# Optimization experiments

Hardware: AMD Instinct MI355X
Metric: run time of the kernel (lower is better)

The kernel has to match this reference:

```python
import jax, jax.numpy as jnp
import numpy as np

B, N, H, W, C = 512, 16, 84, 84, 3
CNN_OUT, ATTN, GH, HEADS, POS, A_DIM = 256, 64, 128, 2, 3, 3
IN_GAT = CNN_OUT + POS  # 259
FLAT = 64 * 16 * 16     # conv output flat dim for 84x84 input


def setup_inputs() -> dict:
    key = jax.random.key(0)
    ks = jax.random.split(key, 16)
    s = 0.05
    return dict(
        cam=jax.random.uniform(ks[0], (B, H, W, C), jnp.float32),
        pos=jax.random.normal(ks[1], (B, POS), jnp.float32),
        team_pos=jax.random.normal(ks[2], (B, N, POS), jnp.float32) * 10.0,
        agent_idx=jax.random.randint(ks[3], (B,), 0, N),
        W1=jax.random.normal(ks[4], (32, C, 8, 8), jnp.float32) * s, b1=jnp.zeros((32,), jnp.float32),
        W2=jax.random.normal(ks[5], (64, 32, 4, 4), jnp.float32) * s, b2=jnp.zeros((64,), jnp.float32),
        W3=jax.random.normal(ks[6], (64, 64, 3, 3), jnp.float32) * s, b3=jnp.zeros((64,), jnp.float32),
        Wp=jax.random.normal(ks[7], (FLAT, CNN_OUT), jnp.float32) * 0.01, bp=jnp.zeros((CNN_OUT,), jnp.float32),
        Wid=jax.random.normal(ks[8], (1, ATTN), jnp.float32) * s, bid=jnp.zeros((ATTN,), jnp.float32),
        Wg=jax.random.normal(ks[9], (IN_GAT, HEADS * GH), jnp.float32) * s,
        a_src=jax.random.normal(ks[10], (HEADS, GH), jnp.float32) * s,
        a_dst=jax.random.normal(ks[11], (HEADS, GH), jnp.float32) * s,
        Wh1=jax.random.normal(ks[12], (HEADS * GH + ATTN, 256), jnp.float32) * s, bh1=jnp.zeros((256,), jnp.float32),
        Wh2=jax.random.normal(ks[13], (256, 2 * A_DIM), jnp.float32) * s, bh2=jnp.zeros((2 * A_DIM,), jnp.float32),
    )


def _conv(x, w, b, stride):
    y = jax.lax.conv_general_dilated(x, w, (stride, stride), 'VALID',
                                     dimension_numbers=('NCHW', 'OIHW', 'NCHW'))
    return jax.nn.relu(y + b[None, :, None, None])


def reference(cam, pos, team_pos, agent_idx, W1, b1, W2, b2, W3, b3, Wp, bp,
              Wid, bid, Wg, a_src, a_dst, Wh1, bh1, Wh2, bh2):
    # CNN encoder (NHWC -> NCHW)
    x = jnp.transpose(cam, (0, 3, 1, 2))
    x = _conv(x, W1, b1, 2)   # [B,32,39,39]
    x = _conv(x, W2, b2, 2)   # [B,64,18,18]
    x = _conv(x, W3, b3, 1)   # [B,64,16,16]
    cam_feat = jax.nn.relu(x.reshape(x.shape[0], -1) @ Wp + bp)  # [B,256]

    # per-node features: broadcast ego cam feat + relative team positions
    rel_pos = team_pos - pos[:, None, :]                                     # [B,N,3]
    node_feats = jnp.concatenate(
        [jnp.broadcast_to(cam_feat[:, None, :], (B, N, CNN_OUT)), rel_pos], axis=-1)  # [B,N,259]

    # adjacency: within 100m, no self-loops, self-loop added for isolated nodes
    dist = jnp.linalg.norm(team_pos[:, :, None, :] - team_pos[:, None, :, :], axis=-1)  # [B,N,N]
    eye = jnp.eye(N, dtype=node_feats.dtype)
    adj = (dist < 100.0).astype(node_feats.dtype) * (1.0 - eye)
    need_self = (adj.sum(axis=2) == 0).astype(adj.dtype)                     # [B,N]
    adj = adj + eye[None] * need_self[..., None]

    # dense multi-head GAT layer
    hN = (node_feats @ Wg).reshape(B, N, HEADS, GH)                          # [B,N,H,D]
    src = jnp.einsum('bnhd,hd->bnh', hN, a_src)
    dst = jnp.einsum('bnhd,hd->bnh', hN, a_dst)
    e = jax.nn.leaky_relu(src[:, :, None, :] + dst[:, None, :, :], 0.2)      # [B,i,j,H]
    e = jnp.where(adj[..., None] > 0, e, -1e9)
    alpha = jax.nn.softmax(e, axis=2)
    h = jnp.einsum('bijh,bjhd->bihd', alpha, hN).reshape(B, N, HEADS * GH)   # [B,N,256]
    h = jax.nn.elu(h)
    h = jnp.nan_to_num(h, nan=0.0, posinf=0.0, neginf=0.0)

    # agent-id embedding, fuse, gather own node, policy head
    id_emb = jax.nn.relu(agent_idx.astype(jnp.float32)[:, None] @ Wid + bid)  # [B,64]
    fused = jnp.concatenate([h, jnp.broadcast_to(id_emb[:, None, :], (B, N, ATTN))], axis=-1)  # [B,N,320]
    agent_feat = fused[jnp.arange(B), agent_idx]                             # [B,320]
    z = jax.nn.relu(agent_feat @ Wh1 + bh1)
    logits = z @ Wh2 + bh2                                                    # [B,6]
    return logits
```

## Files before the change

kernel.cpp:

```cpp
#include <hip/hip_runtime.h>


typedef __attribute__((ext_vector_type(8))) short bf16x8;
typedef __attribute__((ext_vector_type(4))) float f32x4;

union U4 { uint4 v; unsigned int u[4]; bf16x8 h; };

__device__ __forceinline__ unsigned short f2bf(float x) {
    unsigned int u = __float_as_uint(x);
    return (unsigned short)((u + 0x7FFFu + ((u >> 16) & 1u)) >> 16);
}
__device__ __forceinline__ unsigned int pack2(float lo, float hi) {
    return (unsigned int)f2bf(lo) | ((unsigned int)f2bf(hi) << 16);
}
__device__ __forceinline__ bf16x8 loadA(const unsigned int* __restrict__ W, int k8, int M, int oc) {
    U4 r; r.v = *(const uint4*)(W + (((size_t)k8 * M + oc) << 2));
    return r.h;
}
__device__ __forceinline__ bf16x8 loadB(const unsigned int* __restrict__ p, size_t BC) {
    U4 r; r.u[0] = p[0]; r.u[1] = p[BC]; r.u[2] = p[2 * BC]; r.u[3] = p[3 * BC];
    return r.h;
}
#define MFMA(a, b, c) __builtin_amdgcn_mfma_f32_16x16x32_bf16((a), (b), (c), 0, 0, 0)

__device__ __forceinline__ int xcd_swz(int L, int nwg) {
    int q = nwg >> 3, r = nwg & 7;
    int x = L & 7, i = L >> 3;
    return (x < r ? x * (q + 1) : r * (q + 1) + (x - r) * q) + i;
}

__global__ __launch_bounds__(256) void prepack(
    const float* __restrict__ W1, const float* __restrict__ W2,
    const float* __restrict__ W3, const float* __restrict__ Wp,
    const float* __restrict__ Wg, const float* __restrict__ Wh1,
    unsigned int* __restrict__ W1t, unsigned int* __restrict__ W2t,
    unsigned int* __restrict__ W3t, unsigned int* __restrict__ Wpt,
    unsigned int* __restrict__ Wgt, unsigned int* __restrict__ Wh1t)
{
    int i = blockIdx.x * 256 + threadIdx.x;
    if (i < 3072) {
        int j2 = i & 3, oc = (i >> 2) & 31, k8 = i >> 7;
        int c = k8 >> 3, kh = k8 & 7, kw = 2 * j2;
        const float* s = W1 + ((oc * 3 + c) * 8 + kh) * 8;
        W1t[i] = pack2(s[kw], s[kw + 1]);
    } else if (i < 19456) {
        int j = i - 3072;
        int j2 = j & 3, oc = (j >> 2) & 63, k8 = j >> 8;
        int tap = k8 >> 2, ic = (k8 & 3) * 8 + 2 * j2;
        int kh = tap >> 2, kw = tap & 3;
        float a = W2[((oc * 32 + ic) * 4 + kh) * 4 + kw];
        float b = W2[((oc * 32 + ic + 1) * 4 + kh) * 4 + kw];
        W2t[j] = pack2(a, b);
    } else if (i < 37888) {
        int j = i - 19456;
        int j2 = j & 3, oc = (j >> 2) & 63, k8 = j >> 8;
        int tap = k8 >> 3, ic = (k8 & 7) * 8 + 2 * j2;
        int kh = tap / 3, kw = tap % 3;
        float a = W3[((oc * 64 + ic) * 3 + kh) * 3 + kw];
        float b = W3[((oc * 64 + ic + 1) * 3 + kh) * 3 + kw];
        W3t[j] = pack2(a, b);
    } else if (i < 2135040) {
        int j = i - 37888;
        int j2 = j & 3, n = (j >> 2) & 255, k8 = j >> 10;
        int s3 = k8 >> 3, oc = (k8 & 7) * 8 + 2 * j2;
        float a = Wp[(size_t)(oc * 256 + s3) * 256 + n];
        float b = Wp[(size_t)((oc + 1) * 256 + s3) * 256 + n];
        Wpt[j] = pack2(a, b);
    } else if (i < 2167808) {
        int j = i - 2135040;
        int j2 = j & 3, m = (j >> 2) & 255, k8 = j >> 10;
        int k = k8 * 8 + 2 * j2;
        Wgt[j] = pack2(Wg[k * 256 + m], Wg[(k + 1) * 256 + m]);
    } else if (i < 2208768) {
        int j = i - 2167808;
        int j2 = j & 3, m = (j >> 2) & 255, k8 = j >> 10;
        int k = k8 * 8 + 2 * j2;
        Wh1t[j] = pack2(Wh1[k * 256 + m], Wh1[(k + 1) * 256 + m]);
    }
}

__global__ __launch_bounds__(256) void transpose_cam(
    const float* __restrict__ cam, unsigned int* __restrict__ camt, int b0, int BC)
{
    __shared__ float lds[32][253];
    int yy = blockIdx.x;
    int bb = blockIdx.y * 32;
    int t = threadIdx.x;
    for (int f = t; f < 8064; f += 256) {
        int b = f / 252, p = f - b * 252;
        lds[b][p] = cam[(size_t)(b0 + bb + b) * 21168 + yy * 252 + p];
    }
    __syncthreads();
    for (int g = t; g < 4032; g += 256) {
        int b = g & 31, q = g >> 5;
        int c = q / 42, x2 = q - c * 42;
        unsigned int v = pack2(lds[b][6 * x2 + c], lds[b][6 * x2 + 3 + c]);
        camt[(size_t)((c * 84 + yy) * 42 + x2) * BC + bb + b] = v;
    }
}

__global__ __launch_bounds__(256) void conv1_mfma(
    const unsigned int* __restrict__ in32, const unsigned int* __restrict__ Wt,
    const float* __restrict__ bias, unsigned int* __restrict__ out32, int BC, int bqShift)
{
    int wgid = xcd_swz(blockIdx.x, gridDim.x);
    int bq = wgid & ((1 << bqShift) - 1);
    int s = wgid >> bqShift;
    int oh = s / 39, ow = s - oh * 39;
    int wv = threadIdx.x >> 6, l = threadIdx.x & 63;
    int lg = l >> 4, lc = l & 15;
    const size_t sBC = (size_t)BC;
    size_t bcol = (size_t)bq * 128 + wv * 32 + lc;
    f32x4 acc[2][2] = {};
    int ybase = 2 * oh;
    #pragma unroll
    for (int sp = 0; sp < 3; sp++) {
        const int s0 = 2 * sp, s1 = s0 + 1;
        bf16x8 A0[2], A1[2], B0[2], B1[2];
        #pragma unroll
        for (int m = 0; m < 2; m++) {
            A0[m] = loadA(Wt, s0 * 4 + lg, 32, m * 16 + lc);
            A1[m] = loadA(Wt, s1 * 4 + lg, 32, m * 16 + lc);
        }
        const unsigned int* p0 = in32 + (size_t)((sp * 84 + ybase + lg) * 42 + ow) * sBC + bcol;
        const unsigned int* p1 = in32 + (size_t)((sp * 84 + ybase + 4 + lg) * 42 + ow) * sBC + bcol;
        B0[0] = loadB(p0, sBC); B0[1] = loadB(p0 + 16, sBC);
        B1[0] = loadB(p1, sBC); B1[1] = loadB(p1 + 16, sBC);
        #pragma unroll
        for (int m = 0; m < 2; m++) {
            acc[m][0] = MFMA(A0[m], B0[0], acc[m][0]);
            acc[m][1] = MFMA(A0[m], B0[1], acc[m][1]);
            acc[m][0] = MFMA(A1[m], B1[0], acc[m][0]);
            acc[m][1] = MFMA(A1[m], B1[1], acc[m][1]);
        }
    }
    #pragma unroll
    for (int m = 0; m < 2; m++) {
        float4 bv = *(const float4*)(bias + m * 16 + lg * 4);
        #pragma unroll
        for (int g = 0; g < 2; g++) {
            f32x4 a = acc[m][g];
            unsigned int u0 = pack2(fmaxf(a.x + bv.x, 0.f), fmaxf(a.y + bv.y, 0.f));
            unsigned int u1 = pack2(fmaxf(a.z + bv.z, 0.f), fmaxf(a.w + bv.w, 0.f));
            size_t o = (size_t)(s * 16 + m * 8 + lg * 2) * sBC
                     + (size_t)bq * 128 + wv * 32 + g * 16 + lc;
            out32[o] = u0; out32[o + sBC] = u1;
        }
    }
}

__global__ __launch_bounds__(256) void conv2_mfma(
    const unsigned int* __restrict__ in32, const unsigned int* __restrict__ Wt,
    const float* __restrict__ bias, unsigned int* __restrict__ out32, int BC, int bqShift)
{
    int wgid = xcd_swz(blockIdx.x, gridDim.x);
    int bq = wgid & ((1 << bqShift) - 1);
    int s = wgid >> bqShift;
    int oh = s / 18, ow = s - oh * 18;
    int wv = threadIdx.x >> 6, l = threadIdx.x & 63;
    int lg = l >> 4, lc = l & 15;
    const size_t sBC = (size_t)BC;
    size_t bcol = (size_t)bq * 128 + wv * 32 + lc;
    f32x4 acc[4][2] = {};
    int ybase = 2 * oh, xbase = 2 * ow;
    #pragma unroll
    for (int sp = 0; sp < 8; sp++) {
        const int s0 = 2 * sp, s1 = s0 + 1;
        bf16x8 A0[4], A1[4], B0[2], B1[2];
        #pragma unroll
        for (int m = 0; m < 4; m++) {
            A0[m] = loadA(Wt, s0 * 4 + lg, 64, m * 16 + lc);
            A1[m] = loadA(Wt, s1 * 4 + lg, 64, m * 16 + lc);
        }
        {
            const int kh = s0 >> 2, kw = s0 & 3;
            const unsigned int* p = in32
                + (size_t)((((ybase + kh) * 39 + xbase + kw) * 16) + lg * 4) * sBC + bcol;
            B0[0] = loadB(p, sBC); B0[1] = loadB(p + 16, sBC);
        }
        {
            const int kh = s1 >> 2, kw = s1 & 3;
            const unsigned int* p = in32
                + (size_t)((((ybase + kh) * 39 + xbase + kw) * 16) + lg * 4) * sBC + bcol;
            B1[0] = loadB(p, sBC); B1[1] = loadB(p + 16, sBC);
        }
        #pragma unroll
        for (int m = 0; m < 4; m++) {
            acc[m][0] = MFMA(A0[m], B0[0], acc[m][0]);
            acc[m][1] = MFMA(A0[m], B0[1], acc[m][1]);
        }
        #pragma unroll
        for (int m = 0; m < 4; m++) {
            acc[m][0] = MFMA(A1[m], B1[0], acc[m][0]);
            acc[m][1] = MFMA(A1[m], B1[1], acc[m][1]);
        }
    }
    #pragma unroll
    for (int m = 0; m < 4; m++) {
        float4 bv = *(const float4*)(bias + m * 16 + lg * 4);
        #pragma unroll
        for (int g = 0; g < 2; g++) {
            f32x4 a = acc[m][g];
            unsigned int u0 = pack2(fmaxf(a.x + bv.x, 0.f), fmaxf(a.y + bv.y, 0.f));
            unsigned int u1 = pack2(fmaxf(a.z + bv.z, 0.f), fmaxf(a.w + bv.w, 0.f));
            size_t o = (size_t)(s * 32 + m * 8 + lg * 2) * sBC
                     + (size_t)bq * 128 + wv * 32 + g * 16 + lc;
            out32[o] = u0; out32[o + sBC] = u1;
        }
    }
}

__global__ __launch_bounds__(256) void conv3_mfma(
    const unsigned int* __restrict__ in32, const unsigned int* __restrict__ Wt,
    const float* __restrict__ bias, unsigned int* __restrict__ out32, int BC, int bqShift)
{
    int wgid = xcd_swz(blockIdx.x, gridDim.x);
    int bq = wgid & ((1 << bqShift) - 1);
    int s = wgid >> bqShift;
    int oh = s >> 4, ow = s & 15;
    int wv = threadIdx.x >> 6, l = threadIdx.x & 63;
    int lg = l >> 4, lc = l & 15;
    const size_t sBC = (size_t)BC;
    size_t bcol = (size_t)bq * 128 + wv * 32 + lc;
    f32x4 acc[4][2] = {};
    #pragma unroll
    for (int sp = 0; sp < 9; sp++) {
        const int s0 = 2 * sp, s1 = s0 + 1;
        const int kh = sp / 3, kw = sp - kh * 3;
        bf16x8 A0[4], A1[4], B0[2], B1[2];
        #pragma unroll
        for (int m = 0; m < 4; m++) {
            A0[m] = loadA(Wt, s0 * 4 + lg, 64, m * 16 + lc);
            A1[m] = loadA(Wt, s1 * 4 + lg, 64, m * 16 + lc);
        }
        const unsigned int* pb = in32 + (size_t)((((oh + kh) * 18 + ow + kw) * 32)) * sBC;
        const unsigned int* p0 = pb + (size_t)(lg * 4) * sBC + bcol;
        const unsigned int* p1 = pb + (size_t)((4 + lg) * 4) * sBC + bcol;
        B0[0] = loadB(p0, sBC); B0[1] = loadB(p0 + 16, sBC);
        B1[0] = loadB(p1, sBC); B1[1] = loadB(p1 + 16, sBC);
        #pragma unroll
        for (int m = 0; m < 4; m++) {
            acc[m][0] = MFMA(A0[m], B0[0], acc[m][0]);
            acc[m][1] = MFMA(A0[m], B0[1], acc[m][1]);
        }
        #pragma unroll
        for (int m = 0; m < 4; m++) {
            acc[m][0] = MFMA(A1[m], B1[0], acc[m][0]);
            acc[m][1] = MFMA(A1[m], B1[1], acc[m][1]);
        }
    }
    #pragma unroll
    for (int m = 0; m < 4; m++) {
        float4 bv = *(const float4*)(bias + m * 16 + lg * 4);
        #pragma unroll
        for (int g = 0; g < 2; g++) {
            f32x4 a = acc[m][g];
            unsigned int u0 = pack2(fmaxf(a.x + bv.x, 0.f), fmaxf(a.y + bv.y, 0.f));
            unsigned int u1 = pack2(fmaxf(a.z + bv.z, 0.f), fmaxf(a.w + bv.w, 0.f));
            size_t o = (size_t)(s * 32 + m * 8 + lg * 2) * sBC
                     + (size_t)bq * 128 + wv * 32 + g * 16 + lc;
            out32[o] = u0; out32[o + sBC] = u1;
        }
    }
}

__global__ __launch_bounds__(256) void proj_mfma(
    const unsigned int* __restrict__ x3, const unsigned int* __restrict__ Wpt,
    float* __restrict__ partial, int BC, int bqShift)
{
    int wgid = xcd_swz(blockIdx.x, gridDim.x);
    int bq = wgid & ((1 << bqShift) - 1);
    int rem = wgid >> bqShift;
    int mq = rem & 3;
    int kseg = rem >> 2;
    int wv = threadIdx.x >> 6, l = threadIdx.x & 63;
    int lg = l >> 4, lc = l & 15;
    const size_t sBC = (size_t)BC;
    size_t bcol = (size_t)bq * 128 + wv * 32 + lc;
    f32x4 acc[4][2] = {};
    #pragma unroll
    for (int sp = 0; sp < 8; sp++) {
        const int s0 = 2 * sp, s1 = s0 + 1;
        const int s3 = kseg * 8 + sp;
        bf16x8 A0[4], A1[4], B0[2], B1[2];
        #pragma unroll
        for (int m = 0; m < 4; m++) {
            A0[m] = loadA(Wpt, kseg * 64 + s0 * 4 + lg, 256, mq * 64 + m * 16 + lc);
            A1[m] = loadA(Wpt, kseg * 64 + s1 * 4 + lg, 256, mq * 64 + m * 16 + lc);
        }
        const unsigned int* pb = x3 + (size_t)(s3 * 32) * sBC;
        const unsigned int* p0 = pb + (size_t)(lg * 4) * sBC + bcol;
        const unsigned int* p1 = pb + (size_t)((4 + lg) * 4) * sBC + bcol;
        B0[0] = loadB(p0, sBC); B0[1] = loadB(p0 + 16, sBC);
        B1[0] = loadB(p1, sBC); B1[1] = loadB(p1 + 16, sBC);
        #pragma unroll
        for (int m = 0; m < 4; m++) {
            acc[m][0] = MFMA(A0[m], B0[0], acc[m][0]);
            acc[m][1] = MFMA(A0[m], B0[1], acc[m][1]);
        }
        #pragma unroll
        for (int m = 0; m < 4; m++) {
            acc[m][0] = MFMA(A1[m], B1[0], acc[m][0]);
            acc[m][1] = MFMA(A1[m], B1[1], acc[m][1]);
        }
    }
    #pragma unroll
    for (int m = 0; m < 4; m++) {
        #pragma unroll
        for (int g = 0; g < 2; g++) {
            f32x4 a = acc[m][g];
            float* pp = partial
                + (size_t)(kseg * 256 + mq * 64 + m * 16 + lg * 4) * sBC
                + (size_t)bq * 128 + wv * 32 + g * 16 + lc;
            pp[0] = a.x; pp[sBC] = a.y; pp[2 * sBC] = a.z; pp[3 * sBC] = a.w;
        }
    }
}

__global__ __launch_bounds__(256) void reduce_k(
    const float* __restrict__ partial, const float* __restrict__ bp,
    unsigned int* __restrict__ cf16, int b0, int BC, int bcShift)
{
    int i = blockIdx.x * 256 + threadIdx.x;
    int bl = i & (BC - 1);
    int q = i >> bcShift;
    float s0 = 0.f, s1 = 0.f;
    int n0 = 2 * q;
    for (int seg = 0; seg < 32; seg++) {
        s0 += partial[((size_t)(seg * 256 + n0) << bcShift) + bl];
        s1 += partial[((size_t)(seg * 256 + n0 + 1) << bcShift) + bl];
    }
    float v0 = fmaxf(s0 + bp[n0], 0.f);
    float v1 = fmaxf(s1 + bp[n0 + 1], 0.f);
    cf16[(size_t)q * 512 + b0 + bl] = pack2(v0, v1);
}

__global__ __launch_bounds__(64) void gat_prep(
    const unsigned int* __restrict__ cf16, const unsigned int* __restrict__ Wgt,
    float* __restrict__ hNb)
{
    int mq = blockIdx.x, bq = blockIdx.y;
    int l = threadIdx.x, lg = l >> 4, lc = l & 15;
    size_t bcol = (size_t)bq * 32 + lc;
    f32x4 acc[4][2] = {};
    #pragma unroll
    for (int sp = 0; sp < 4; sp++) {
        const int s0 = 2 * sp, s1 = s0 + 1;
        bf16x8 A0[4], A1[4], B0[2], B1[2];
        #pragma unroll
        for (int m = 0; m < 4; m++) {
            A0[m] = loadA(Wgt, s0 * 4 + lg, 256, mq * 64 + m * 16 + lc);
            A1[m] = loadA(Wgt, s1 * 4 + lg, 256, mq * 64 + m * 16 + lc);
        }
        const unsigned int* p0 = cf16 + (size_t)(sp * 32 + lg * 4) * 512 + bcol;
        const unsigned int* p1 = p0 + (size_t)16 * 512;
        B0[0] = loadB(p0, 512); B0[1] = loadB(p0 + 16, 512);
        B1[0] = loadB(p1, 512); B1[1] = loadB(p1 + 16, 512);
        #pragma unroll
        for (int m = 0; m < 4; m++) {
            acc[m][0] = MFMA(A0[m], B0[0], acc[m][0]);
            acc[m][1] = MFMA(A0[m], B0[1], acc[m][1]);
        }
        #pragma unroll
        for (int m = 0; m < 4; m++) {
            acc[m][0] = MFMA(A1[m], B1[0], acc[m][0]);
            acc[m][1] = MFMA(A1[m], B1[1], acc[m][1]);
        }
    }
    #pragma unroll
    for (int m = 0; m < 4; m++) {
        #pragma unroll
        for (int g = 0; g < 2; g++) {
            size_t b = (size_t)bq * 32 + g * 16 + lc;
            int row0 = mq * 64 + m * 16 + lg * 4;
            *(f32x4*)(hNb + b * 256 + row0) = acc[m][g];
        }
    }
}

__global__ __launch_bounds__(256) void gat_mid(
    const float* __restrict__ hNb, const float* __restrict__ pos,
    const float* __restrict__ tpos, const int* __restrict__ aidx,
    const float* __restrict__ Wg, const float* __restrict__ asrc, const float* __restrict__ adst,
    const float* __restrict__ Wid, const float* __restrict__ bid,
    unsigned int* __restrict__ af16)
{
    int b = blockIdx.x, t = threadIdx.x;
    __shared__ float hN[16][256];
    __shared__ float srcv[16][2], dstv[16][2];
    __shared__ float alpha[16][2];
    __shared__ float af[320];
    __shared__ unsigned int adjm_s;

    int ai = aidx[b];
    float basev = hNb[(size_t)b * 256 + t];
    float rw0 = Wg[65536 + t], rw1 = Wg[65792 + t], rw2 = Wg[66048 + t];
    float px = pos[b * 3 + 0], py = pos[b * 3 + 1], pz = pos[b * 3 + 2];
    for (int n = 0; n < 16; n++) {
        float r0 = tpos[(b * 16 + n) * 3 + 0] - px;
        float r1 = tpos[(b * 16 + n) * 3 + 1] - py;
        float r2 = tpos[(b * 16 + n) * 3 + 2] - pz;
        hN[n][t] = basev + r0 * rw0 + r1 * rw1 + r2 * rw2;
    }

    if (t < 64) {
        bool on = false;
        if (t < 16 && t != ai) {
            float dx = tpos[(b * 16 + ai) * 3 + 0] - tpos[(b * 16 + t) * 3 + 0];
            float dy = tpos[(b * 16 + ai) * 3 + 1] - tpos[(b * 16 + t) * 3 + 1];
            float dz = tpos[(b * 16 + ai) * 3 + 2] - tpos[(b * 16 + t) * 3 + 2];
            on = (dx * dx + dy * dy + dz * dz) < 10000.0f;
        }
        unsigned long long m = __ballot(on);
        if (t == 0) adjm_s = (m == 0ull) ? (1u << ai) : (unsigned int)m;
    }
    __syncthreads();

    {
        int p = t >> 3, sub = t & 7;
        int j = p >> 1, h = p & 1;
        float s1 = 0.f, s2 = 0.f;
        #pragma unroll
        for (int dd = 0; dd < 16; dd++) {
            int d = h * 128 + sub * 16 + dd;
            float v = hN[j][d];
            s1 += v * asrc[d];
            s2 += v * adst[d];
        }
        s1 += __shfl_xor(s1, 1); s1 += __shfl_xor(s1, 2); s1 += __shfl_xor(s1, 4);
        s2 += __shfl_xor(s2, 1); s2 += __shfl_xor(s2, 2); s2 += __shfl_xor(s2, 4);
        if (sub == 0) { srcv[j][h] = s1; dstv[j][h] = s2; }
    }
    __syncthreads();

    if (t < 32) {
        int j = t & 15, h = t >> 4;
        unsigned int am = adjm_s;
        float e = srcv[ai][h] + dstv[j][h];
        e = (e > 0.f) ? e : 0.2f * e;
        e = ((am >> j) & 1u) ? e : -1e9f;
        float mx = e;
        mx = fmaxf(mx, __shfl_xor(mx, 1));
        mx = fmaxf(mx, __shfl_xor(mx, 2));
        mx = fmaxf(mx, __shfl_xor(mx, 4));
        mx = fmaxf(mx, __shfl_xor(mx, 8));
        float ex = __expf(e - mx);
        float sm = ex;
        sm += __shfl_xor(sm, 1); sm += __shfl_xor(sm, 2);
        sm += __shfl_xor(sm, 4); sm += __shfl_xor(sm, 8);
        alpha[j][h] = ex / sm;
    }
    __syncthreads();

    {
        int h = t >> 7;
        float o = 0.f;
        #pragma unroll
        for (int j = 0; j < 16; j++) o += alpha[j][h] * hN[j][t];
        o = (o > 0.f) ? o : (__expf(o) - 1.f);
        af[t] = o;
    }
    if (t < 64) {
        float v = (float)ai * Wid[t] + bid[t];
        af[256 + t] = fmaxf(v, 0.f);
    }
    __syncthreads();

    if (t < 160) af16[(size_t)t * 512 + b] = pack2(af[2 * t], af[2 * t + 1]);
}

__global__ __launch_bounds__(64) void head_mfma(
    const unsigned int* __restrict__ af16, const unsigned int* __restrict__ Wh1t,
    const float* __restrict__ bh1, float* __restrict__ zf)
{
    int mq = blockIdx.x, bq = blockIdx.y;
    int l = threadIdx.x, lg = l >> 4, lc = l & 15;
    size_t bcol = (size_t)bq * 32 + lc;
    f32x4 acc[4][2] = {};
    #pragma unroll
    for (int sp = 0; sp < 5; sp++) {
        const int s0 = 2 * sp, s1 = s0 + 1;
        bf16x8 A0[4], A1[4], B0[2], B1[2];
        #pragma unroll
        for (int m = 0; m < 4; m++) {
            A0[m] = loadA(Wh1t, s0 * 4 + lg, 256, mq * 64 + m * 16 + lc);
            A1[m] = loadA(Wh1t, s1 * 4 + lg, 256, mq * 64 + m * 16 + lc);
        }
        const unsigned int* p0 = af16 + (size_t)(sp * 32 + lg * 4) * 512 + bcol;
        const unsigned int* p1 = p0 + (size_t)16 * 512;
        B0[0] = loadB(p0, 512); B0[1] = loadB(p0 + 16, 512);
        B1[0] = loadB(p1, 512); B1[1] = loadB(p1 + 16, 512);
        #pragma unroll
        for (int m = 0; m < 4; m++) {
            acc[m][0] = MFMA(A0[m], B0[0], acc[m][0]);
            acc[m][1] = MFMA(A0[m], B0[1], acc[m][1]);
        }
        #pragma unroll
        for (int m = 0; m < 4; m++) {
            acc[m][0] = MFMA(A1[m], B1[0], acc[m][0]);
            acc[m][1] = MFMA(A1[m], B1[1], acc[m][1]);
        }
    }
    #pragma unroll
    for (int m = 0; m < 4; m++) {
        int row0 = mq * 64 + m * 16 + lg * 4;
        float4 bv = *(const float4*)(bh1 + row0);
        #pragma unroll
        for (int g = 0; g < 2; g++) {
            f32x4 a = acc[m][g];
            size_t b = (size_t)bq * 32 + g * 16 + lc;
            float* pp = zf + (size_t)row0 * 512 + b;
            pp[0]        = fmaxf(a.x + bv.x, 0.f);
            pp[512]      = fmaxf(a.y + bv.y, 0.f);
            pp[2 * 512]  = fmaxf(a.z + bv.z, 0.f);
            pp[3 * 512]  = fmaxf(a.w + bv.w, 0.f);
        }
    }
}

__global__ __launch_bounds__(256) void logits_k(
    const float* __restrict__ zf, const float* __restrict__ Wh2,
    const float* __restrict__ bh2, float* __restrict__ out)
{
    __shared__ float Ws[1536];
    int t = threadIdx.x;
    int b = blockIdx.x * 256 + t;
    for (int f = t; f < 1536; f += 256) Ws[f] = Wh2[f];
    __syncthreads();
    float acc[6];
    #pragma unroll
    for (int j = 0; j < 6; j++) acc[j] = bh2[j];
    for (int k = 0; k < 256; k++) {
        float zv = zf[(size_t)k * 512 + b];
        #pragma unroll
        for (int j = 0; j < 6; j++) acc[j] += zv * Ws[k * 6 + j];
    }
    #pragma unroll
    for (int j = 0; j < 6; j++) out[b * 6 + j] = acc[j];
}

extern "C" void kernel_launch(void* const* d_in, const int* in_sizes, int n_in,
                              void* d_out, int out_size, void* d_ws, size_t ws_size,
                              hipStream_t stream)
{
    const float* cam  = (const float*)d_in[0];
    const float* pos  = (const float*)d_in[1];
    const float* tpos = (const float*)d_in[2];
    const int*   aidx = (const int*)d_in[3];
    const float* W1   = (const float*)d_in[4];
    const float* b1   = (const float*)d_in[5];
    const float* W2   = (const float*)d_in[6];
    const float* b2   = (const float*)d_in[7];
    const float* W3   = (const float*)d_in[8];
    const float* b3   = (const float*)d_in[9];
    const float* Wp   = (const float*)d_in[10];
    const float* bp   = (const float*)d_in[11];
    const float* Wid  = (const float*)d_in[12];
    const float* bid  = (const float*)d_in[13];
    const float* Wg   = (const float*)d_in[14];
    const float* asrc = (const float*)d_in[15];
    const float* adst = (const float*)d_in[16];
    const float* Wh1  = (const float*)d_in[17];
    const float* bh1  = (const float*)d_in[18];
    const float* Wh2  = (const float*)d_in[19];
    const float* bh2  = (const float*)d_in[20];
    float* out = (float*)d_out;

    int BC = 128;
    {
        const int cands[3] = {512, 256, 128};
        for (int idx = 0; idx < 3; idx++) {
            size_t need = ((size_t)51304 * cands[idx] + 2618368) * 4;
            if (need <= ws_size) { BC = cands[idx]; break; }
        }
    }
    int bcShift = (BC == 512) ? 9 : (BC == 256) ? 8 : 7;
    int nbq = BC >> 7;
    int bqShift = (BC == 512) ? 2 : (BC == 256) ? 1 : 0;

    unsigned int* ws32 = (unsigned int*)d_ws;
    unsigned int* RA  = ws32;
    unsigned int* RB  = RA + (size_t)10584 * BC;
    unsigned int* RC  = RB + (size_t)24336 * BC;
    float*        RD  = (float*)(RC + (size_t)8192 * BC);
    unsigned int* W1t = (unsigned int*)(RD + (size_t)8192 * BC);
    unsigned int* W2t  = W1t + 3072;
    unsigned int* W3t  = W2t + 16384;
    unsigned int* Wpt  = W3t + 18432;
    unsigned int* Wgt  = Wpt + 2097152;
    unsigned int* Wh1t = Wgt + 32768;
    unsigned int* cf16 = Wh1t + 40960;
    float*        hNb  = (float*)(cf16 + 65536);
    unsigned int* af16 = (unsigned int*)(hNb + 131072);
    float*        zf   = (float*)(af16 + 81920);

    prepack<<<8628, 256, 0, stream>>>(W1, W2, W3, Wp, Wg, Wh1,
                                      W1t, W2t, W3t, Wpt, Wgt, Wh1t);

    for (int b0 = 0; b0 < 512; b0 += BC) {
        transpose_cam<<<dim3(84, BC / 32), 256, 0, stream>>>(cam, RA, b0, BC);
        conv1_mfma<<<1521 * nbq, 256, 0, stream>>>(RA, W1t, b1, RB, BC, bqShift);
        conv2_mfma<<<324 * nbq, 256, 0, stream>>>(RB, W2t, b2, RA, BC, bqShift);
        conv3_mfma<<<256 * nbq, 256, 0, stream>>>(RA, W3t, b3, RC, BC, bqShift);
        proj_mfma<<<128 * nbq, 256, 0, stream>>>(RC, Wpt, RD, BC, bqShift);
        reduce_k<<<BC / 2, 256, 0, stream>>>(RD, bp, cf16, b0, BC, bcShift);
    }
    gat_prep<<<dim3(4, 16), 64, 0, stream>>>(cf16, Wgt, hNb);
    gat_mid<<<512, 256, 0, stream>>>(hNb, pos, tpos, aidx, Wg, asrc, adst,
                                     Wid, bid, af16);
    head_mfma<<<dim3(4, 16), 64, 0, stream>>>(af16, Wh1t, bh1, zf);
    logits_k<<<2, 256, 0, stream>>>(zf, Wh2, bh2, out);
}
```

Before: 163.5 us.

## Switch activations to k8-packed layout with 16-byte loads and wider per-wave batch tiles

```diff
diff --git a/kernel.cpp b/kernel.cpp
--- a/kernel.cpp
+++ b/kernel.cpp
@@ -17,7 +17,11 @@
     U4 r; r.v = *(const uint4*)(W + (((size_t)k8 * M + oc) << 2));
     return r.h;
 }
-__device__ __forceinline__ bf16x8 loadB(const unsigned int* __restrict__ p, size_t BC) {
+__device__ __forceinline__ bf16x8 loadB4(const unsigned int* __restrict__ base, size_t idx) {
+    U4 r; r.v = *(const uint4*)(base + (idx << 2));
+    return r.h;
+}
+__device__ __forceinline__ bf16x8 loadBp(const unsigned int* __restrict__ p, size_t BC) {
     U4 r; r.u[0] = p[0]; r.u[1] = p[BC]; r.u[2] = p[2 * BC]; r.u[3] = p[3 * BC];
     return r.h;
 }
@@ -27,6 +31,13 @@
     int q = nwg >> 3, r = nwg & 7;
     int x = L & 7, i = L >> 3;
     return (x < r ? x * (q + 1) : r * (q + 1) + (x - r) * q) + i;
+}
+
+__device__ __forceinline__ void storeK(unsigned int* __restrict__ out,
+                                       size_t row, size_t BC, size_t bcol,
+                                       int lg, unsigned int u0, unsigned int u1) {
+    uint2 v; v.x = u0; v.y = u1;
+    *(uint2*)(out + ((row * BC + bcol) << 2) + ((lg & 1) << 1)) = v;
 }
 
 __global__ __launch_bounds__(256) void prepack(
@@ -101,72 +112,79 @@
 
 __global__ __launch_bounds__(256) void conv1_mfma(
     const unsigned int* __restrict__ in32, const unsigned int* __restrict__ Wt,
-    const float* __restrict__ bias, unsigned int* __restrict__ out32, int BC, int bqShift)
+    const float* __restrict__ bias, unsigned int* __restrict__ out32,
+    int BC, int nspat)
 {
     int wgid = xcd_swz(blockIdx.x, gridDim.x);
-    int bq = wgid & ((1 << bqShift) - 1);
-    int s = wgid >> bqShift;
+    int s = wgid % nspat;
+    int bq = wgid / nspat;
     int oh = s / 39, ow = s - oh * 39;
     int wv = threadIdx.x >> 6, l = threadIdx.x & 63;
     int lg = l >> 4, lc = l & 15;
     const size_t sBC = (size_t)BC;
-    size_t bcol = (size_t)bq * 128 + wv * 32 + lc;
-    f32x4 acc[2][2] = {};
+    size_t base = (size_t)bq * 256 + wv * 64 + lc;
+    f32x4 acc[2][4] = {};
     int ybase = 2 * oh;
     #pragma unroll
     for (int sp = 0; sp < 3; sp++) {
         const int s0 = 2 * sp, s1 = s0 + 1;
-        bf16x8 A0[2], A1[2], B0[2], B1[2];
+        bf16x8 A0[2], A1[2], B0[4], B1[4];
         #pragma unroll
         for (int m = 0; m < 2; m++) {
             A0[m] = loadA(Wt, s0 * 4 + lg, 32, m * 16 + lc);
             A1[m] = loadA(Wt, s1 * 4 + lg, 32, m * 16 + lc);
         }
-        const unsigned int* p0 = in32 + (size_t)((sp * 84 + ybase + lg) * 42 + ow) * sBC + bcol;
-        const unsigned int* p1 = in32 + (size_t)((sp * 84 + ybase + 4 + lg) * 42 + ow) * sBC + bcol;
-        B0[0] = loadB(p0, sBC); B0[1] = loadB(p0 + 16, sBC);
-        B1[0] = loadB(p1, sBC); B1[1] = loadB(p1 + 16, sBC);
-        #pragma unroll
-        for (int m = 0; m < 2; m++) {
-            acc[m][0] = MFMA(A0[m], B0[0], acc[m][0]);
-            acc[m][1] = MFMA(A0[m], B0[1], acc[m][1]);
-            acc[m][0] = MFMA(A1[m], B1[0], acc[m][0]);
-            acc[m][1] = MFMA(A1[m], B1[1], acc[m][1]);
-        }
+        const unsigned int* p0 = in32 + (size_t)((sp * 84 + ybase + lg) * 42 + ow) * sBC + base;
+        const unsigned int* p1 = in32 + (size_t)((sp * 84 + ybase + 4 + lg) * 42 + ow) * sBC + base;
+        #pragma unroll
+        for (int g = 0; g < 4; g++) {
+            B0[g] = loadBp(p0 + g * 16, sBC);
+            B1[g] = loadBp(p1 + g * 16, sBC);
+        }
+        #pragma unroll
+        for (int m = 0; m < 2; m++)
+            #pragma unroll
+            for (int g = 0; g < 4; g++)
+                acc[m][g] = MFMA(A0[m], B0[g], acc[m][g]);
+        #pragma unroll
+        for (int m = 0; m < 2; m++)
+            #pragma unroll
+            for (int g = 0; g < 4; g++)
+                acc[m][g] = MFMA(A1[m], B1[g], acc[m][g]);
     }
     #pragma unroll
     for (int m = 0; m < 2; m++) {
         float4 bv = *(const float4*)(bias + m * 16 + lg * 4);
-        #pragma unroll
-        for (int g = 0; g < 2; g++) {
+        size_t row = (size_t)s * 4 + 2 * m + (lg >> 1);
+        #pragma unroll
+        for (int g = 0; g < 4; g++) {
             f32x4 a = acc[m][g];
             unsigned int u0 = pack2(fmaxf(a.x + bv.x, 0.f), fmaxf(a.y + bv.y, 0.f));
             unsigned int u1 = pack2(fmaxf(a.z + bv.z, 0.f), fmaxf(a.w + bv.w, 0.f));
-            size_t o = (size_t)(s * 16 + m * 8 + lg * 2) * sBC
-                     + (size_t)bq * 128 + wv * 32 + g * 16 + lc;
-            out32[o] = u0; out32[o + sBC] = u1;
+            storeK(out32, row, sBC, base + g * 16, lg, u0, u1);
         }
     }
 }
 
 __global__ __launch_bounds__(256) void conv2_mfma(
     const unsigned int* __restrict__ in32, const unsigned int* __restrict__ Wt,
-    const float* __restrict__ bias, unsigned int* __restrict__ out32, int BC, int bqShift)
+    const float* __restrict__ bias, unsigned int* __restrict__ out32,
+    int BC, int nspat)
 {
     int wgid = xcd_swz(blockIdx.x, gridDim.x);
-    int bq = wgid & ((1 << bqShift) - 1);
-    int s = wgid >> bqShift;
+    int s = wgid % nspat;
+    int bq = wgid / nspat;
     int oh = s / 18, ow = s - oh * 18;
     int wv = threadIdx.x >> 6, l = threadIdx.x & 63;
     int lg = l >> 4, lc = l & 15;
     const size_t sBC = (size_t)BC;
-    size_t bcol = (size_t)bq * 128 + wv * 32 + lc;
-    f32x4 acc[4][2] = {};
+    size_t base = (size_t)bq * 256 + wv * 64 + lc;
+    f32x4 acc[4][4] = {};
     int ybase = 2 * oh, xbase = 2 * ow;
     #pragma unroll
     for (int sp = 0; sp < 8; sp++) {
         const int s0 = 2 * sp, s1 = s0 + 1;
-        bf16x8 A0[4], A1[4], B0[2], B1[2];
+        bf16x8 A0[4], A1[4], B0[4], B1[4];
         #pragma unroll
         for (int m = 0; m < 4; m++) {
             A0[m] = loadA(Wt, s0 * 4 + lg, 64, m * 16 + lc);
@@ -174,146 +192,143 @@
         }
         {
             const int kh = s0 >> 2, kw = s0 & 3;
-            const unsigned int* p = in32
-                + (size_t)((((ybase + kh) * 39 + xbase + kw) * 16) + lg * 4) * sBC + bcol;
-            B0[0] = loadB(p, sBC); B0[1] = loadB(p + 16, sBC);
+            size_t row = (size_t)(((ybase + kh) * 39 + xbase + kw) * 4 + lg);
+            #pragma unroll
+            for (int g = 0; g < 4; g++)
+                B0[g] = loadB4(in32, row * sBC + base + g * 16);
         }
         {
             const int kh = s1 >> 2, kw = s1 & 3;
-            const unsigned int* p = in32
-                + (size_t)((((ybase + kh) * 39 + xbase + kw) * 16) + lg * 4) * sBC + bcol;
-            B1[0] = loadB(p, sBC); B1[1] = loadB(p + 16, sBC);
-        }
-        #pragma unroll
-        for (int m = 0; m < 4; m++) {
-            acc[m][0] = MFMA(A0[m], B0[0], acc[m][0]);
-            acc[m][1] = MFMA(A0[m], B0[1], acc[m][1]);
-        }
-        #pragma unroll
-        for (int m = 0; m < 4; m++) {
-            acc[m][0] = MFMA(A1[m], B1[0], acc[m][0]);
-            acc[m][1] = MFMA(A1[m], B1[1], acc[m][1]);
-        }
+            size_t row = (size_t)(((ybase + kh) * 39 + xbase + kw) * 4 + lg);
+            #pragma unroll
+            for (int g = 0; g < 4; g++)
+                B1[g] = loadB4(in32, row * sBC + base + g * 16);
+        }
+        #pragma unroll
+        for (int m = 0; m < 4; m++)
+            #pragma unroll
+            for (int g = 0; g < 4; g++)
+                acc[m][g] = MFMA(A0[m], B0[g], acc[m][g]);
+        #pragma unroll
+        for (int m = 0; m < 4; m++)
+            #pragma unroll
+            for (int g = 0; g < 4; g++)
+                acc[m][g] = MFMA(A1[m], B1[g], acc[m][g]);
     }
     #pragma unroll
     for (int m = 0; m < 4; m++) {
         float4 bv = *(const float4*)(bias + m * 16 + lg * 4);
-        #pragma unroll
-        for (int g = 0; g < 2; g++) {
+        size_t row = (size_t)s * 8 + 2 * m + (lg >> 1);
+        #pragma unroll
+        for (int g = 0; g < 4; g++) {
             f32x4 a = acc[m][g];
             unsigned int u0 = pack2(fmaxf(a.x + bv.x, 0.f), fmaxf(a.y + bv.y, 0.f));
             unsigned int u1 = pack2(fmaxf(a.z + bv.z, 0.f), fmaxf(a.w + bv.w, 0.f));
-            size_t o = (size_t)(s * 32 + m * 8 + lg * 2) * sBC
-                     + (size_t)bq * 128 + wv * 32 + g * 16 + lc;
-            out32[o] = u0; out32[o + sBC] = u1;
+            storeK(out32, row, sBC, base + g * 16, lg, u0, u1);
         }
     }
 }
 
 __global__ __launch_bounds__(256) void conv3_mfma(
     const unsigned int* __restrict__ in32, const unsigned int* __restrict__ Wt,
-    const float* __restrict__ bias, unsigned int* __restrict__ out32, int BC, int bqShift)
+    const float* __restrict__ bias, unsigned int* __restrict__ out32,
+    int BC, int nspat)
 {
     int wgid = xcd_swz(blockIdx.x, gridDim.x);
-    int bq = wgid & ((1 << bqShift) - 1);
-    int s = wgid >> bqShift;
+    int s = wgid % nspat;
+    int bq = wgid / nspat;
     int oh = s >> 4, ow = s & 15;
     int wv = threadIdx.x >> 6, l = threadIdx.x & 63;
     int lg = l >> 4, lc = l & 15;
     const size_t sBC = (size_t)BC;
-    size_t bcol = (size_t)bq * 128 + wv * 32 + lc;
-    f32x4 acc[4][2] = {};
+    size_t base = (size_t)bq * 256 + wv * 64 + lc;
+    f32x4 acc[4][4] = {};
     #pragma unroll
     for (int sp = 0; sp < 9; sp++) {
         const int s0 = 2 * sp, s1 = s0 + 1;
         const int kh = sp / 3, kw = sp - kh * 3;
-        bf16x8 A0[4], A1[4], B0[2], B1[2];
+        bf16x8 A0[4], A1[4], B0[4], B1[4];
         #pragma unroll
         for (int m = 0; m < 4; m++) {
             A0[m] = loadA(Wt, s0 * 4 + lg, 64, m * 16 + lc);
             A1[m] = loadA(Wt, s1 * 4 + lg, 64, m * 16 + lc);
         }
-        const unsigned int* pb = in32 + (size_t)((((oh + kh) * 18 + ow + kw) * 32)) * sBC;
-        const unsigned int* p0 = pb + (size_t)(lg * 4) * sBC + bcol;
-        const unsigned int* p1 = pb + (size_t)((4 + lg) * 4) * sBC + bcol;
-        B0[0] = loadB(p0, sBC); B0[1] = loadB(p0 + 16, sBC);
-        B1[0] = loadB(p1, sBC); B1[1] = loadB(p1 + 16, sBC);
-        #pragma unroll
-        for (int m = 0; m < 4; m++) {
-            acc[m][0] = MFMA(A0[m], B0[0], acc[m][0]);
-            acc[m][1] = MFMA(A0[m], B0[1], acc[m][1]);
-        }
-        #pragma unroll
-        for (int m = 0; m < 4; m++) {
-            acc[m][0] = MFMA(A1[m], B1[0], acc[m][0]);
-            acc[m][1] = MFMA(A1[m], B1[1], acc[m][1]);
-        }
+        size_t row0 = (size_t)(((oh + kh) * 18 + ow + kw) * 8 + lg);
+        #pragma unroll
+        for (int g = 0; g < 4; g++) {
+            B0[g] = loadB4(in32, row0 * sBC + base + g * 16);
+            B1[g] = loadB4(in32, (row0 + 4) * sBC + base + g * 16);
+        }
+        #pragma unroll
+        for (int m = 0; m < 4; m++)
+            #pragma unroll
+            for (int g = 0; g < 4; g++)
+                acc[m][g] = MFMA(A0[m], B0[g], acc[m][g]);
+        #pragma unroll
+        for (int m = 0; m < 4; m++)
+            #pragma unroll
+            for (int g = 0; g < 4; g++)
+                acc[m][g] = MFMA(A1[m], B1[g], acc[m][g]);
     }
     #pragma unroll
     for (int m = 0; m < 4; m++) {
         float4 bv = *(const float4*)(bias + m * 16 + lg * 4);
-        #pragma unroll
-        for (int g = 0; g < 2; g++) {
+        size_t row = (size_t)s * 8 + 2 * m + (lg >> 1);
+        #pragma unroll
+        for (int g = 0; g < 4; g++) {
             f32x4 a = acc[m][g];
             unsigned int u0 = pack2(fmaxf(a.x + bv.x, 0.f), fmaxf(a.y + bv.y, 0.f));
             unsigned int u1 = pack2(fmaxf(a.z + bv.z, 0.f), fmaxf(a.w + bv.w, 0.f));
-            size_t o = (size_t)(s * 32 + m * 8 + lg * 2) * sBC
-                     + (size_t)bq * 128 + wv * 32 + g * 16 + lc;
-            out32[o] = u0; out32[o + sBC] = u1;
+            storeK(out32, row, sBC, base + g * 16, lg, u0, u1);
         }
     }
 }
 
 __global__ __launch_bounds__(256) void proj_mfma(
     const unsigned int* __restrict__ x3, const unsigned int* __restrict__ Wpt,
-    float* __restrict__ partial, int BC, int bqShift)
+    float* __restrict__ partial, int BC)
 {
     int wgid = xcd_swz(blockIdx.x, gridDim.x);
-    int bq = wgid & ((1 << bqShift) - 1);
-    int rem = wgid >> bqShift;
+    int rem = wgid & 127;
+    int bq = wgid >> 7;
     int mq = rem & 3;
     int kseg = rem >> 2;
     int wv = threadIdx.x >> 6, l = threadIdx.x & 63;
     int lg = l >> 4, lc = l & 15;
     const size_t sBC = (size_t)BC;
-    size_t bcol = (size_t)bq * 128 + wv * 32 + lc;
-    f32x4 acc[4][2] = {};
+    size_t base = (size_t)bq * 256 + wv * 64 + lc;
+    f32x4 acc[4][4] = {};
     #pragma unroll
     for (int sp = 0; sp < 8; sp++) {
-        const int s0 = 2 * sp, s1 = s0 + 1;
-        const int s3 = kseg * 8 + sp;
-        bf16x8 A0[4], A1[4], B0[2], B1[2];
+        const int k8b = kseg * 64 + sp * 8;
+        bf16x8 A0[4], A1[4], B0[4], B1[4];
         #pragma unroll
         for (int m = 0; m < 4; m++) {
-            A0[m] = loadA(Wpt, kseg * 64 + s0 * 4 + lg, 256, mq * 64 + m * 16 + lc);
-            A1[m] = loadA(Wpt, kseg * 64 + s1 * 4 + lg, 256, mq * 64 + m * 16 + lc);
-        }
-        const unsigned int* pb = x3 + (size_t)(s3 * 32) * sBC;
-        const unsigned int* p0 = pb + (size_t)(lg * 4) * sBC + bcol;
-        const unsigned int* p1 = pb + (size_t)((4 + lg) * 4) * sBC + bcol;
-        B0[0] = loadB(p0, sBC); B0[1] = loadB(p0 + 16, sBC);
-        B1[0] = loadB(p1, sBC); B1[1] = loadB(p1 + 16, sBC);
-        #pragma unroll
-        for (int m = 0; m < 4; m++) {
-            acc[m][0] = MFMA(A0[m], B0[0], acc[m][0]);
-            acc[m][1] = MFMA(A0[m], B0[1], acc[m][1]);
-        }
-        #pragma unroll
-        for (int m = 0; m < 4; m++) {
-            acc[m][0] = MFMA(A1[m], B1[0], acc[m][0]);
-            acc[m][1] = MFMA(A1[m], B1[1], acc[m][1]);
-        }
+            A0[m] = loadA(Wpt, k8b + lg, 256, mq * 64 + m * 16 + lc);
+            A1[m] = loadA(Wpt, k8b + 4 + lg, 256, mq * 64 + m * 16 + lc);
+        }
+        #pragma unroll
+        for (int g = 0; g < 4; g++) {
+            B0[g] = loadB4(x3, (size_t)(k8b + lg) * sBC + base + g * 16);
+            B1[g] = loadB4(x3, (size_t)(k8b + 4 + lg) * sBC + base + g * 16);
+        }
+        #pragma unroll
+        for (int m = 0; m < 4; m++)
+            #pragma unroll
+            for (int g = 0; g < 4; g++)
+                acc[m][g] = MFMA(A0[m], B0[g], acc[m][g]);
+        #pragma unroll
+        for (int m = 0; m < 4; m++)
+            #pragma unroll
+            for (int g = 0; g < 4; g++)
+                acc[m][g] = MFMA(A1[m], B1[g], acc[m][g]);
     }
     #pragma unroll
     for (int m = 0; m < 4; m++) {
-        #pragma unroll
-        for (int g = 0; g < 2; g++) {
-            f32x4 a = acc[m][g];
-            float* pp = partial
-                + (size_t)(kseg * 256 + mq * 64 + m * 16 + lg * 4) * sBC
-                + (size_t)bq * 128 + wv * 32 + g * 16 + lc;
-            pp[0] = a.x; pp[sBC] = a.y; pp[2 * sBC] = a.z; pp[3 * sBC] = a.w;
-        }
+        size_t row4 = (size_t)kseg * 64 + mq * 16 + m * 4 + lg;
+        #pragma unroll
+        for (int g = 0; g < 4; g++)
+            *(f32x4*)(partial + ((row4 * sBC + base + g * 16) << 2)) = acc[m][g];
     }
 }
 
@@ -323,16 +338,20 @@
 {
     int i = blockIdx.x * 256 + threadIdx.x;
     int bl = i & (BC - 1);
-    int q = i >> bcShift;
-    float s0 = 0.f, s1 = 0.f;
-    int n0 = 2 * q;
+    int k8 = i >> bcShift;
+    f32x4 S0 = {}, S1 = {};
     for (int seg = 0; seg < 32; seg++) {
-        s0 += partial[((size_t)(seg * 256 + n0) << bcShift) + bl];
-        s1 += partial[((size_t)(seg * 256 + n0 + 1) << bcShift) + bl];
-    }
-    float v0 = fmaxf(s0 + bp[n0], 0.f);
-    float v1 = fmaxf(s1 + bp[n0 + 1], 0.f);
-    cf16[(size_t)q * 512 + b0 + bl] = pack2(v0, v1);
+        const float* p = partial + (((size_t)(seg * 64 + k8 * 2) * BC + bl) << 2);
+        S0 += *(const f32x4*)p;
+        S1 += *(const f32x4*)(p + (BC << 2));
+    }
+    int n = k8 * 8;
+    uint4 u;
+    u.x = pack2(fmaxf(S0.x + bp[n + 0], 0.f), fmaxf(S0.y + bp[n + 1], 0.f));
+    u.y = pack2(fmaxf(S0.z + bp[n + 2], 0.f), fmaxf(S0.w + bp[n + 3], 0.f));
+    u.z = pack2(fmaxf(S1.x + bp[n + 4], 0.f), fmaxf(S1.y + bp[n + 5], 0.f));
+    u.w = pack2(fmaxf(S1.z + bp[n + 6], 0.f), fmaxf(S1.w + bp[n + 7], 0.f));
+    *(uint4*)(cf16 + (((size_t)k8 * 512 + b0 + bl) << 2)) = u;
 }
 
 __global__ __launch_bounds__(64) void gat_prep(
@@ -352,17 +371,15 @@
             A0[m] = loadA(Wgt, s0 * 4 + lg, 256, mq * 64 + m * 16 + lc);
             A1[m] = loadA(Wgt, s1 * 4 + lg, 256, mq * 64 + m * 16 + lc);
         }
-        const unsigned int* p0 = cf16 + (size_t)(sp * 32 + lg * 4) * 512 + bcol;
-        const unsigned int* p1 = p0 + (size_t)16 * 512;
-        B0[0] = loadB(p0, 512); B0[1] = loadB(p0 + 16, 512);
-        B1[0] = loadB(p1, 512); B1[1] = loadB(p1 + 16, 512);
+        #pragma unroll
+        for (int g = 0; g < 2; g++) {
+            B0[g] = loadB4(cf16, (size_t)(s0 * 4 + lg) * 512 + bcol + g * 16);
+            B1[g] = loadB4(cf16, (size_t)(s1 * 4 + lg) * 512 + bcol + g * 16);
+        }
         #pragma unroll
         for (int m = 0; m < 4; m++) {
             acc[m][0] = MFMA(A0[m], B0[0], acc[m][0]);
             acc[m][1] = MFMA(A0[m], B0[1], acc[m][1]);
-        }
-        #pragma unroll
-        for (int m = 0; m < 4; m++) {
             acc[m][0] = MFMA(A1[m], B1[0], acc[m][0]);
             acc[m][1] = MFMA(A1[m], B1[1], acc[m][1]);
         }
@@ -466,7 +483,14 @@
     }
     __syncthreads();
 
-    if (t < 160) af16[(size_t)t * 512 + b] = pack2(af[2 * t], af[2 * t + 1]);
+    if (t < 40) {
+        uint4 u;
+        u.x = pack2(af[t * 8 + 0], af[t * 8 + 1]);
+        u.y = pack2(af[t * 8 + 2], af[t * 8 + 3]);
+        u.z = pack2(af[t * 8 + 4], af[t * 8 + 5]);
+        u.w = pack2(af[t * 8 + 6], af[t * 8 + 7]);
+        *(uint4*)(af16 + (((size_t)t * 512 + b) << 2)) = u;
+    }
 }
 
 __global__ __launch_bounds__(64) void head_mfma(
@@ -486,17 +510,15 @@
             A0[m] = loadA(Wh1t, s0 * 4 + lg, 256, mq * 64 + m * 16 + lc);
             A1[m] = loadA(Wh1t, s1 * 4 + lg, 256, mq * 64 + m * 16 + lc);
         }
-        const unsigned int* p0 = af16 + (size_t)(sp * 32 + lg * 4) * 512 + bcol;
-        const unsigned int* p1 = p0 + (size_t)16 * 512;
-        B0[0] = loadB(p0, 512); B0[1] = loadB(p0 + 16, 512);
-        B1[0] = loadB(p1, 512); B1[1] = loadB(p1 + 16, 512);
+        #pragma unroll
+        for (int g = 0; g < 2; g++) {
+            B0[g] = loadB4(af16, (size_t)(s0 * 4 + lg) * 512 + bcol + g * 16);
+            B1[g] = loadB4(af16, (size_t)(s1 * 4 + lg) * 512 + bcol + g * 16);
+        }
         #pragma unroll
         for (int m = 0; m < 4; m++) {
             acc[m][0] = MFMA(A0[m], B0[0], acc[m][0]);
             acc[m][1] = MFMA(A0[m], B0[1], acc[m][1]);
-        }
-        #pragma unroll
-        for (int m = 0; m < 4; m++) {
             acc[m][0] = MFMA(A1[m], B1[0], acc[m][0]);
             acc[m][1] = MFMA(A1[m], B1[1], acc[m][1]);
         }
@@ -510,10 +532,10 @@
             f32x4 a = acc[m][g];
             size_t b = (size_t)bq * 32 + g * 16 + lc;
             float* pp = zf + (size_t)row0 * 512 + b;
-            pp[0]        = fmaxf(a.x + bv.x, 0.f);
-            pp[512]      = fmaxf(a.y + bv.y, 0.f);
-            pp[2 * 512]  = fmaxf(a.z + bv.z, 0.f);
-            pp[3 * 512]  = fmaxf(a.w + bv.w, 0.f);
+            pp[0]       = fmaxf(a.x + bv.x, 0.f);
+            pp[512]     = fmaxf(a.y + bv.y, 0.f);
+            pp[2 * 512] = fmaxf(a.z + bv.z, 0.f);
+            pp[3 * 512] = fmaxf(a.w + bv.w, 0.f);
         }
     }
 }
@@ -566,17 +588,10 @@
     const float* bh2  = (const float*)d_in[20];
     float* out = (float*)d_out;
 
-    int BC = 128;
-    {
-        const int cands[3] = {512, 256, 128};
-        for (int idx = 0; idx < 3; idx++) {
-            size_t need = ((size_t)51304 * cands[idx] + 2618368) * 4;
-            if (need <= ws_size) { BC = cands[idx]; break; }
-        }
-    }
-    int bcShift = (BC == 512) ? 9 : (BC == 256) ? 8 : 7;
-    int nbq = BC >> 7;
-    int bqShift = (BC == 512) ? 2 : (BC == 256) ? 1 : 0;
+    int BC = 256;
+    if (((size_t)51304 * 512 + 2618368) * 4 <= ws_size) BC = 512;
+    int bcShift = (BC == 512) ? 9 : 8;
+    int nbq2 = BC >> 8;
 
     unsigned int* ws32 = (unsigned int*)d_ws;
     unsigned int* RA  = ws32;
@@ -599,11 +614,11 @@
 
     for (int b0 = 0; b0 < 512; b0 += BC) {
         transpose_cam<<<dim3(84, BC / 32), 256, 0, stream>>>(cam, RA, b0, BC);
-        conv1_mfma<<<1521 * nbq, 256, 0, stream>>>(RA, W1t, b1, RB, BC, bqShift);
-        conv2_mfma<<<324 * nbq, 256, 0, stream>>>(RB, W2t, b2, RA, BC, bqShift);
-        conv3_mfma<<<256 * nbq, 256, 0, stream>>>(RA, W3t, b3, RC, BC, bqShift);
-        proj_mfma<<<128 * nbq, 256, 0, stream>>>(RC, Wpt, RD, BC, bqShift);
-        reduce_k<<<BC / 2, 256, 0, stream>>>(RD, bp, cf16, b0, BC, bcShift);
+        conv1_mfma<<<1521 * nbq2, 256, 0, stream>>>(RA, W1t, b1, RB, BC, 1521);
+        conv2_mfma<<<324 * nbq2, 256, 0, stream>>>(RB, W2t, b2, RA, BC, 324);
+        conv3_mfma<<<256 * nbq2, 256, 0, stream>>>(RA, W3t, b3, RC, BC, 256);
+        proj_mfma<<<128 * nbq2, 256, 0, stream>>>(RC, Wpt, RD, BC);
+        reduce_k<<<(32 * BC) / 256, 256, 0, stream>>>(RD, bp, cf16, b0, BC, bcShift);
     }
     gat_prep<<<dim3(4, 16), 64, 0, stream>>>(cf16, Wgt, hNb);
     gat_mid<<<512, 256, 0, stream>>>(hNb, pos, tpos, aidx, Wg, asrc, adst,
```

Result: faster. 147.6 us (-9.7%).
